# Kernel tuning notes

Hardware: AMD Instinct MI355X
Metric: run time of the kernel (lower is better)

## Reference

```python
import jax, jax.numpy as jnp
import numpy as np

S = 7
B = 2
CLS = 20
N = CLS + B * 5  # 30
LAMBDA_COORD = 5.0
LAMBDA_NOOBJ = 0.5
BATCH = 16384


def setup_inputs() -> dict:
    key = jax.random.key(0)
    k1, k2, k3 = jax.random.split(key, 3)
    pred = jax.random.uniform(k1, (BATCH, S, S, N), dtype=jnp.float32)
    target = jax.random.uniform(k2, (BATCH, S, S, N), dtype=jnp.float32)
    # conf channel (index 4) must be exactly 0 or 1 -- it drives the obj/noobj masks
    obj = (jax.random.uniform(k3, (BATCH, S, S)) < 0.15).astype(jnp.float32)
    target = target.at[..., 4].set(obj)
    return {"pred": pred, "target": target}


def _iou(b1, b2):
    # b1: [M, B, 4] xyxy, b2: [M, 4] xyxy -> [M, B]
    lt = jnp.maximum(b1[..., :2], b2[:, None, :2])
    rb = jnp.minimum(b1[..., 2:], b2[:, None, 2:])
    wh = jnp.clip(rb - lt, 0.0)
    inter = wh[..., 0] * wh[..., 1]
    area1 = (b1[..., 2] - b1[..., 0]) * (b1[..., 3] - b1[..., 1])
    area2 = ((b2[:, 2] - b2[:, 0]) * (b2[:, 3] - b2[:, 1]))[:, None]
    union = area1 + area2 - inter
    return jnp.where(union > 0, inter / union, 0.0)


def reference(pred, target):
    batch = pred.shape[0]
    p = pred.reshape(-1, N)   # [M, 30], M = batch*S*S
    t = target.reshape(-1, N)
    obj = (t[:, 4] == 1).astype(pred.dtype)    # positive-cell mask
    noobj = (t[:, 4] == 0).astype(pred.dtype)  # negative-cell mask

    # faithful to source: conf_loc = arange(B)*B + 4 -> [4, 6]
    conf_loc = jnp.arange(B) * B + 4
    noobj_conf_loss = jnp.sum(noobj[:, None] * (p[:, conf_loc] - t[:, conf_loc]) ** 2)

    pb = p[:, : B * 5].reshape(-1, B, 5)  # [M, B, 5] (x, y, w, h, conf)
    tb = t[:, :5]                         # [M, 5] first target box per cell

    # xywh -> xyxy
    pb_xyxy = jnp.concatenate([pb[..., :2] - pb[..., 2:4] / 2,
                               pb[..., :2] + pb[..., 2:4] / 2], axis=-1)
    tb_xyxy = jnp.concatenate([tb[:, :2] - tb[:, 2:4] / 2,
                               tb[:, :2] + tb[:, 2:4] / 2], axis=-1)

    iou = _iou(pb_xyxy, tb_xyxy)                         # [M, B]
    j = jnp.argmax(iou, axis=1)                          # responsible box index
    max_iou = jax.lax.stop_gradient(jnp.max(iou, axis=1))
    resp = jnp.take_along_axis(pb, j[:, None, None], axis=1)[:, 0]  # [M, 5]

    xy_loss = jnp.sum((resp[:, :2] - tb[:, :2]) ** 2, axis=-1)
    wh_loss = jnp.sum((jnp.sqrt(jnp.clip(resp[:, 2:4], 0.0))
                       - jnp.sqrt(jnp.clip(tb[:, 2:4], 0.0))) ** 2, axis=-1)
    coord_loss = jnp.sum(obj * (xy_loss + wh_loss))

    obj_conf_loss = jnp.sum(obj * (resp[:, 4] - max_iou) ** 2)
    class_loss = jnp.sum(obj[:, None] * (p[:, B * 5:] - t[:, B * 5:]) ** 2)

    total = (LAMBDA_COORD * coord_loss + obj_conf_loss
             + LAMBDA_NOOBJ * noobj_conf_loss + class_loss) / batch
    return total
```

## Files before the change

kernel.cpp:

```cpp
#include <hip/hip_runtime.h>


#define TPB 256
#define CELLS 256
#define CB 30720
#define GRID 3136

__global__ __launch_bounds__(TPB, 2) void yolo_loss_kernel(
    const float* __restrict__ pred, const float* __restrict__ target,
    float* __restrict__ out)
{
    __shared__ __align__(16) unsigned char smem[2 * CB];
    __shared__ float red[TPB / 64];

    const int tid = threadIdx.x;
    const size_t base = (size_t)blockIdx.x * CB;

    const char* gp = (const char*)pred + base;
    const char* gt = (const char*)target + base;
    float4 vp[7], vt[7];
    float2 wp, wt;
    #pragma unroll
    for (int i = 0; i < 7; i++) vp[i] = *(const float4*)(gp + i * 4096 + tid * 16);
    wp = *(const float2*)(gp + 28672 + tid * 8);
    #pragma unroll
    for (int i = 0; i < 7; i++) vt[i] = *(const float4*)(gt + i * 4096 + tid * 16);
    wt = *(const float2*)(gt + 28672 + tid * 8);

    #pragma unroll
    for (int i = 0; i < 7; i++) *(float4*)(smem + i * 4096 + tid * 16) = vp[i];
    *(float2*)(smem + 28672 + tid * 8) = wp;
    #pragma unroll
    for (int i = 0; i < 7; i++) *(float4*)(smem + CB + i * 4096 + tid * 16) = vt[i];
    *(float2*)(smem + CB + 28672 + tid * 8) = wt;
    __syncthreads();

    const float* pf = (const float*)(smem) + tid * 30;
    const float* tf = (const float*)(smem + CB) + tid * 30;

    float sum = 0.0f;
    const float t4 = tf[4];
    if (t4 == 0.0f) {
        float d4 = pf[4] - t4;
        float d6 = pf[6] - tf[6];
        sum = 0.5f * (d4 * d4 + d6 * d6);
    } else if (t4 == 1.0f) {
        float tx1 = tf[0] - tf[2] * 0.5f, ty1 = tf[1] - tf[3] * 0.5f;
        float tx2 = tf[0] + tf[2] * 0.5f, ty2 = tf[1] + tf[3] * 0.5f;
        float area2 = (tx2 - tx1) * (ty2 - ty1);

        float ax1 = pf[0] - pf[2] * 0.5f, ay1 = pf[1] - pf[3] * 0.5f;
        float ax2 = pf[0] + pf[2] * 0.5f, ay2 = pf[1] + pf[3] * 0.5f;
        float w0 = fmaxf(fminf(ax2, tx2) - fmaxf(ax1, tx1), 0.0f);
        float h0 = fmaxf(fminf(ay2, ty2) - fmaxf(ay1, ty1), 0.0f);
        float inter0 = w0 * h0;
        float uni0 = (ax2 - ax1) * (ay2 - ay1) + area2 - inter0;
        float iou0 = (uni0 > 0.0f) ? (inter0 / uni0) : 0.0f;

        float bx1 = pf[5] - pf[7] * 0.5f, by1 = pf[6] - pf[8] * 0.5f;
        float bx2 = pf[5] + pf[7] * 0.5f, by2 = pf[6] + pf[8] * 0.5f;
        float w1 = fmaxf(fminf(bx2, tx2) - fmaxf(bx1, tx1), 0.0f);
        float h1 = fmaxf(fminf(by2, ty2) - fmaxf(by1, ty1), 0.0f);
        float inter1 = w1 * h1;
        float uni1 = (bx2 - bx1) * (by2 - by1) + area2 - inter1;
        float iou1 = (uni1 > 0.0f) ? (inter1 / uni1) : 0.0f;

        bool j1 = (iou1 > iou0);
        float max_iou = fmaxf(iou0, iou1);
        float r0 = j1 ? pf[5] : pf[0];
        float r1 = j1 ? pf[6] : pf[1];
        float r2 = j1 ? pf[7] : pf[2];
        float r3 = j1 ? pf[8] : pf[3];
        float r4 = j1 ? pf[9] : pf[4];

        float dx = r0 - tf[0];
        float dy = r1 - tf[1];
        float sw = sqrtf(fmaxf(r2, 0.0f)) - sqrtf(fmaxf(tf[2], 0.0f));
        float sh = sqrtf(fmaxf(r3, 0.0f)) - sqrtf(fmaxf(tf[3], 0.0f));
        float coord = dx * dx + dy * dy + sw * sw + sh * sh;
        float dc = r4 - max_iou;

        float cls = 0.0f;
        #pragma unroll
        for (int k = 10; k < 30; k++) {
            float d = pf[k] - tf[k];
            cls += d * d;
        }
        sum = 5.0f * coord + dc * dc + cls;
    }

    #pragma unroll
    for (int off = 32; off > 0; off >>= 1)
        sum += __shfl_down(sum, off, 64);
    if ((tid & 63) == 0) red[tid >> 6] = sum;
    __syncthreads();
    if (tid == 0) {
        float s = red[0] + red[1] + red[2] + red[3];
        atomicAdd(out, s * (1.0f / 16384.0f));
    }
}

extern "C" void kernel_launch(void* const* d_in, const int* in_sizes, int n_in,
                              void* d_out, int out_size, void* d_ws, size_t ws_size,
                              hipStream_t stream) {
    const float* pred = (const float*)d_in[0];
    const float* target = (const float*)d_in[1];
    float* out = (float*)d_out;
    hipMemsetAsync(out, 0, sizeof(float), stream);
    yolo_loss_kernel<<<GRID, TPB, 0, stream>>>(pred, target, out);
}
```

Baseline: 204.2 us.

## Use persistent per-wave tiles with register prefetch of the next tile

Replaces the one-block-per-256-cells launch with a fixed grid of 512 persistent blocks. Each wave owns a 64-cell tile, stages it to its private LDS slice without block barriers, and issues the global loads for its next tile before computing the current one. This overlaps memory latency with compute and cuts launch and atomic overhead. The trade-off is fewer blocks in flight (512 across the device), which may expose latency if occupancy is too low, and per-wave LDS reuse relies on in-wave ordering.

```diff
diff --git a/kernel.cpp b/kernel.cpp
--- a/kernel.cpp
+++ b/kernel.cpp
@@ -2,99 +2,127 @@
 
 
 #define TPB 256
-#define CELLS 256
-#define CB 30720
-#define GRID 3136
+#define WPB 4
+#define WCELLS 64
+#define WB (WCELLS * 120)
+#define SLICE (2 * WB)
+#define R_TOTAL (16384 * 7 * 7)
+#define NTILES (R_TOTAL / WCELLS)
+#define GRID 512
+#define NWAVES (GRID * WPB)
 
 __global__ __launch_bounds__(TPB, 2) void yolo_loss_kernel(
     const float* __restrict__ pred, const float* __restrict__ target,
     float* __restrict__ out)
 {
-    __shared__ __align__(16) unsigned char smem[2 * CB];
-    __shared__ float red[TPB / 64];
+    __shared__ __align__(16) unsigned char smem[WPB * SLICE];
+    __shared__ float red[WPB];
 
-    const int tid = threadIdx.x;
-    const size_t base = (size_t)blockIdx.x * CB;
+    const int widx = threadIdx.x >> 6;
+    const int lane = threadIdx.x & 63;
+    unsigned char* slice = smem + widx * SLICE;
 
-    const char* gp = (const char*)pred + base;
-    const char* gt = (const char*)target + base;
     float4 vp[7], vt[7];
     float2 wp, wt;
-    #pragma unroll
-    for (int i = 0; i < 7; i++) vp[i] = *(const float4*)(gp + i * 4096 + tid * 16);
-    wp = *(const float2*)(gp + 28672 + tid * 8);
-    #pragma unroll
-    for (int i = 0; i < 7; i++) vt[i] = *(const float4*)(gt + i * 4096 + tid * 16);
-    wt = *(const float2*)(gt + 28672 + tid * 8);
-
-    #pragma unroll
-    for (int i = 0; i < 7; i++) *(float4*)(smem + i * 4096 + tid * 16) = vp[i];
-    *(float2*)(smem + 28672 + tid * 8) = wp;
-    #pragma unroll
-    for (int i = 0; i < 7; i++) *(float4*)(smem + CB + i * 4096 + tid * 16) = vt[i];
-    *(float2*)(smem + CB + 28672 + tid * 8) = wt;
-    __syncthreads();
-
-    const float* pf = (const float*)(smem) + tid * 30;
-    const float* tf = (const float*)(smem + CB) + tid * 30;
 
     float sum = 0.0f;
-    const float t4 = tf[4];
-    if (t4 == 0.0f) {
-        float d4 = pf[4] - t4;
-        float d6 = pf[6] - tf[6];
-        sum = 0.5f * (d4 * d4 + d6 * d6);
-    } else if (t4 == 1.0f) {
-        float tx1 = tf[0] - tf[2] * 0.5f, ty1 = tf[1] - tf[3] * 0.5f;
-        float tx2 = tf[0] + tf[2] * 0.5f, ty2 = tf[1] + tf[3] * 0.5f;
-        float area2 = (tx2 - tx1) * (ty2 - ty1);
+    size_t t = (size_t)blockIdx.x * WPB + widx;
 
-        float ax1 = pf[0] - pf[2] * 0.5f, ay1 = pf[1] - pf[3] * 0.5f;
-        float ax2 = pf[0] + pf[2] * 0.5f, ay2 = pf[1] + pf[3] * 0.5f;
-        float w0 = fmaxf(fminf(ax2, tx2) - fmaxf(ax1, tx1), 0.0f);
-        float h0 = fmaxf(fminf(ay2, ty2) - fmaxf(ay1, ty1), 0.0f);
-        float inter0 = w0 * h0;
-        float uni0 = (ax2 - ax1) * (ay2 - ay1) + area2 - inter0;
-        float iou0 = (uni0 > 0.0f) ? (inter0 / uni0) : 0.0f;
+    {
+        const char* gp = (const char*)pred + t * (size_t)WB;
+        const char* gt = (const char*)target + t * (size_t)WB;
+        #pragma unroll
+        for (int i = 0; i < 7; i++) vp[i] = *(const float4*)(gp + i * 1024 + lane * 16);
+        wp = *(const float2*)(gp + 7168 + lane * 8);
+        #pragma unroll
+        for (int i = 0; i < 7; i++) vt[i] = *(const float4*)(gt + i * 1024 + lane * 16);
+        wt = *(const float2*)(gt + 7168 + lane * 8);
+    }
 
-        float bx1 = pf[5] - pf[7] * 0.5f, by1 = pf[6] - pf[8] * 0.5f;
-        float bx2 = pf[5] + pf[7] * 0.5f, by2 = pf[6] + pf[8] * 0.5f;
-        float w1 = fmaxf(fminf(bx2, tx2) - fmaxf(bx1, tx1), 0.0f);
-        float h1 = fmaxf(fminf(by2, ty2) - fmaxf(by1, ty1), 0.0f);
-        float inter1 = w1 * h1;
-        float uni1 = (bx2 - bx1) * (by2 - by1) + area2 - inter1;
-        float iou1 = (uni1 > 0.0f) ? (inter1 / uni1) : 0.0f;
+    for (;;) {
+        #pragma unroll
+        for (int i = 0; i < 7; i++) *(float4*)(slice + i * 1024 + lane * 16) = vp[i];
+        *(float2*)(slice + 7168 + lane * 8) = wp;
+        #pragma unroll
+        for (int i = 0; i < 7; i++) *(float4*)(slice + WB + i * 1024 + lane * 16) = vt[i];
+        *(float2*)(slice + WB + 7168 + lane * 8) = wt;
 
-        bool j1 = (iou1 > iou0);
-        float max_iou = fmaxf(iou0, iou1);
-        float r0 = j1 ? pf[5] : pf[0];
-        float r1 = j1 ? pf[6] : pf[1];
-        float r2 = j1 ? pf[7] : pf[2];
-        float r3 = j1 ? pf[8] : pf[3];
-        float r4 = j1 ? pf[9] : pf[4];
+        const size_t tn = t + NWAVES;
+        const bool more = (tn < NTILES);
+        if (more) {
+            const char* gp = (const char*)pred + tn * (size_t)WB;
+            const char* gt = (const char*)target + tn * (size_t)WB;
+            #pragma unroll
+            for (int i = 0; i < 7; i++) vp[i] = *(const float4*)(gp + i * 1024 + lane * 16);
+            wp = *(const float2*)(gp + 7168 + lane * 8);
+            #pragma unroll
+            for (int i = 0; i < 7; i++) vt[i] = *(const float4*)(gt + i * 1024 + lane * 16);
+            wt = *(const float2*)(gt + 7168 + lane * 8);
+        }
 
-        float dx = r0 - tf[0];
-        float dy = r1 - tf[1];
-        float sw = sqrtf(fmaxf(r2, 0.0f)) - sqrtf(fmaxf(tf[2], 0.0f));
-        float sh = sqrtf(fmaxf(r3, 0.0f)) - sqrtf(fmaxf(tf[3], 0.0f));
-        float coord = dx * dx + dy * dy + sw * sw + sh * sh;
-        float dc = r4 - max_iou;
+        const float* pf = (const float*)(slice) + lane * 30;
+        const float* tf = (const float*)(slice + WB) + lane * 30;
 
-        float cls = 0.0f;
-        #pragma unroll
-        for (int k = 10; k < 30; k++) {
-            float d = pf[k] - tf[k];
-            cls += d * d;
+        const float t4 = tf[4];
+        if (t4 == 0.0f) {
+            float d4 = pf[4] - t4;
+            float d6 = pf[6] - tf[6];
+            sum += 0.5f * (d4 * d4 + d6 * d6);
+        } else if (t4 == 1.0f) {
+            float tx1 = tf[0] - tf[2] * 0.5f, ty1 = tf[1] - tf[3] * 0.5f;
+            float tx2 = tf[0] + tf[2] * 0.5f, ty2 = tf[1] + tf[3] * 0.5f;
+            float area2 = (tx2 - tx1) * (ty2 - ty1);
+
+            float ax1 = pf[0] - pf[2] * 0.5f, ay1 = pf[1] - pf[3] * 0.5f;
+            float ax2 = pf[0] + pf[2] * 0.5f, ay2 = pf[1] + pf[3] * 0.5f;
+            float w0 = fmaxf(fminf(ax2, tx2) - fmaxf(ax1, tx1), 0.0f);
+            float h0 = fmaxf(fminf(ay2, ty2) - fmaxf(ay1, ty1), 0.0f);
+            float inter0 = w0 * h0;
+            float uni0 = (ax2 - ax1) * (ay2 - ay1) + area2 - inter0;
+            float iou0 = (uni0 > 0.0f) ? (inter0 / uni0) : 0.0f;
+
+            float bx1 = pf[5] - pf[7] * 0.5f, by1 = pf[6] - pf[8] * 0.5f;
+            float bx2 = pf[5] + pf[7] * 0.5f, by2 = pf[6] + pf[8] * 0.5f;
+            float w1 = fmaxf(fminf(bx2, tx2) - fmaxf(bx1, tx1), 0.0f);
+            float h1 = fmaxf(fminf(by2, ty2) - fmaxf(by1, ty1), 0.0f);
+            float inter1 = w1 * h1;
+            float uni1 = (bx2 - bx1) * (by2 - by1) + area2 - inter1;
+            float iou1 = (uni1 > 0.0f) ? (inter1 / uni1) : 0.0f;
+
+            bool j1 = (iou1 > iou0);
+            float max_iou = fmaxf(iou0, iou1);
+            float r0 = j1 ? pf[5] : pf[0];
+            float r1 = j1 ? pf[6] : pf[1];
+            float r2 = j1 ? pf[7] : pf[2];
+            float r3 = j1 ? pf[8] : pf[3];
+            float r4 = j1 ? pf[9] : pf[4];
+
+            float dx = r0 - tf[0];
+            float dy = r1 - tf[1];
+            float sw = sqrtf(fmaxf(r2, 0.0f)) - sqrtf(fmaxf(tf[2], 0.0f));
+            float sh = sqrtf(fmaxf(r3, 0.0f)) - sqrtf(fmaxf(tf[3], 0.0f));
+            float coord = dx * dx + dy * dy + sw * sw + sh * sh;
+            float dc = r4 - max_iou;
+
+            float cls = 0.0f;
+            #pragma unroll
+            for (int k = 10; k < 30; k++) {
+                float d = pf[k] - tf[k];
+                cls += d * d;
+            }
+            sum += 5.0f * coord + dc * dc + cls;
         }
-        sum = 5.0f * coord + dc * dc + cls;
+
+        if (!more) break;
+        t = tn;
     }
 
     #pragma unroll
     for (int off = 32; off > 0; off >>= 1)
         sum += __shfl_down(sum, off, 64);
-    if ((tid & 63) == 0) red[tid >> 6] = sum;
+    if (lane == 0) red[widx] = sum;
     __syncthreads();
-    if (tid == 0) {
+    if (threadIdx.x == 0) {
         float s = red[0] + red[1] + red[2] + red[3];
         atomicAdd(out, s * (1.0f / 16384.0f));
     }
```

After: 233.0 us. 1.14x slower.
